# Kernel tuning notes

Measured on AMD Instinct MI355X. Metric: run time of the kernel, lower is better.

The kernel has to match this reference:

```python
import jax, jax.numpy as jnp
import numpy as np

NEG_SLOPE = 0.2  # HANConv default negative_slope
N_NODES = 100000
N_REL = 8
N_EDGES = 200000
N_LABEL = 131072
C_IN = 128
H1 = 128
H2 = 128


def _segment_softmax(logits, seg, num_segments):
    # PyG softmax(src, index): exp(src - max_per_seg) / (sum_per_seg + 1e-16)
    m = jax.ops.segment_max(logits, seg, num_segments=num_segments)
    m = jnp.where(jnp.isfinite(m), m, 0.0)  # empty segments -> 0
    e = jnp.exp(logits - m[seg])
    s = jax.ops.segment_sum(e, seg, num_segments=num_segments)
    return e / (s[seg] + 1e-16)


def _han_layer(x, edge_index, proj_w, proj_b, att_src, att_dst, q, klin_w, klin_b):
    # x: [N, Cin]; edge_index: [R, 2, E]; att_src/att_dst: [R, D]; klin_w: [D, D] (torch [out,in])
    N = x.shape[0]
    h = x @ proj_w + proj_b            # [N, D] shared projection for node type 'node'
    a_src = h @ att_src.T              # [N, R] per-node src attention logits
    a_dst = h @ att_dst.T              # [N, R]

    def per_rel(eidx, a_s, a_d):
        src, dst = eidx[0], eidx[1]
        alpha = jax.nn.leaky_relu(a_s[src] + a_d[dst], NEG_SLOPE)     # [E]
        alpha = _segment_softmax(alpha, dst, N)                        # softmax over in-neighbors
        out = jax.ops.segment_sum(alpha[:, None] * h[src], dst, num_segments=N)  # [N, D]
        return jax.nn.relu(out)        # HANConv applies relu per edge-type output

    outs = jax.vmap(per_rel, in_axes=(0, 1, 1))(edge_index, a_src, a_dst)  # [R, N, D]
    # semantic attention across edge types (group())
    score = jnp.einsum('d,rd->r', q, jnp.tanh(outs @ klin_w.T + klin_b).mean(axis=1))
    attn = jax.nn.softmax(score)       # [R]
    return jnp.einsum('r,rnd->nd', attn, outs)


def setup_inputs() -> dict:
    key = jax.random.key(0)
    ks = jax.random.split(key, 24)
    f32 = jnp.float32

    def lin_w(k, fin, fout):
        return (jax.random.normal(k, (fin, fout), f32) / np.sqrt(fin)).astype(f32)

    inp = {
        'x': jax.random.normal(ks[0], (N_NODES, C_IN), f32),
        'edge_index': jax.random.randint(ks[1], (N_REL, 2, N_EDGES), 0, N_NODES, jnp.int32),
        'edge_label_index': jax.random.randint(ks[2], (2, N_LABEL), 0, N_NODES, jnp.int32),
        # HANConv layer 1 params
        'w1': lin_w(ks[3], C_IN, H1), 'b1': jnp.zeros((H1,), f32),
        'asrc1': jax.random.normal(ks[4], (N_REL, H1), f32) / np.sqrt(H1),
        'adst1': jax.random.normal(ks[5], (N_REL, H1), f32) / np.sqrt(H1),
        'q1': jax.random.normal(ks[6], (H1,), f32) / np.sqrt(H1),
        'kw1': lin_w(ks[7], H1, H1).T, 'kb1': jnp.zeros((H1,), f32),
        # HANConv layer 2 params
        'w2': lin_w(ks[8], H1, H2), 'b2': jnp.zeros((H2,), f32),
        'asrc2': jax.random.normal(ks[9], (N_REL, H2), f32) / np.sqrt(H2),
        'adst2': jax.random.normal(ks[10], (N_REL, H2), f32) / np.sqrt(H2),
        'q2': jax.random.normal(ks[11], (H2,), f32) / np.sqrt(H2),
        'kw2': lin_w(ks[12], H2, H2).T, 'kb2': jnp.zeros((H2,), f32),
        # link-score head
        'post_w': lin_w(ks[13], H2, 2), 'post_b': jnp.zeros((2,), f32),
    }
    return inp


def reference(x, edge_index, edge_label_index,
              w1, b1, asrc1, adst1, q1, kw1, kb1,
              w2, b2, asrc2, adst2, q2, kw2, kb2,
              post_w, post_b):
    h = jax.nn.relu(_han_layer(x, edge_index, w1, b1, asrc1, adst1, q1, kw1, kb1))
    h = jax.nn.relu(_han_layer(h, edge_index, w2, b2, asrc2, adst2, q2, kw2, kb2))
    h_had = h[edge_label_index[0]] * h[edge_label_index[1]]   # [L, H2]
    logits = h_had @ post_w + post_b                          # [L, 2]
    return logits.sum(axis=-1)                                # [L]
```

## Files before the change

kernel.cpp:

```cpp
#include <hip/hip_runtime.h>
#include <hip/hip_fp8.h>

#define NN 100000
#define NR 8
#define NE 200000
#define NL 131072
#define NSEG (NR*NN)
#define NB_SCAN 782
#define NPAD (NB_SCAN*1024)

typedef __attribute__((ext_vector_type(8))) short short8;
typedef __attribute__((ext_vector_type(8))) _Float16 half8;
typedef __attribute__((ext_vector_type(4))) float floatx4;

__device__ __forceinline__ unsigned short f2h(float f) {
    _Float16 h = (_Float16)f;
    union { _Float16 h; unsigned short u; } c; c.h = h; return c.u;
}
__device__ __forceinline__ float h2f(unsigned short u) {
    union { _Float16 h; unsigned short u; } c; c.u = u; return (float)c.h;
}
__device__ __forceinline__ unsigned fp8enc(float f) {
    __hip_fp8_e4m3 t(f); return (unsigned)t.__x;
}
__device__ __forceinline__ float fp8dec(unsigned b) {
    __hip_fp8_e4m3 t; t.__x = (__hip_fp8_storage_t)b; return (float)t;
}

#if defined(__has_builtin)
#if __has_builtin(__builtin_amdgcn_cvt_f32_fp8)
#define HW_FP8_DEC 1
#endif
#endif

__device__ __forceinline__ void dec4(unsigned w, float* f) {
#ifdef HW_FP8_DEC
    f[0] = __builtin_amdgcn_cvt_f32_fp8(w, 0);
    f[1] = __builtin_amdgcn_cvt_f32_fp8(w, 1);
    f[2] = __builtin_amdgcn_cvt_f32_fp8(w, 2);
    f[3] = __builtin_amdgcn_cvt_f32_fp8(w, 3);
#else
    f[0] = fp8dec(w & 0xFF);
    f[1] = fp8dec((w >> 8) & 0xFF);
    f[2] = fp8dec((w >> 16) & 0xFF);
    f[3] = fp8dec((w >> 24) & 0xFF);
#endif
}

__global__ void transpose128(const float* __restrict__ in, float* __restrict__ out) {
    int idx = blockIdx.x * 256 + threadIdx.x;
    int j = idx >> 7, k = idx & 127;
    out[idx] = in[k * 128 + j];
}

__global__ void cast_f16(const float* __restrict__ src, unsigned short* __restrict__ dst) {
    size_t idx = ((size_t)blockIdx.x * 256 + threadIdx.x) * 4;
    float4 v = *(const float4*)(src + idx);
    ushort4 o;
    o.x = f2h(v.x); o.y = f2h(v.y); o.z = f2h(v.z); o.w = f2h(v.w);
    *(ushort4*)(dst + idx) = o;
}

__global__ void hist_kernel(const int* __restrict__ ei, int* __restrict__ counts) {
    int idx = blockIdx.x * 256 + threadIdx.x;
    if (idx >= NR * NE) return;
    int r = idx / NE, e = idx - r * NE;
    int dst = ei[(size_t)r * 2 * NE + NE + e];
    atomicAdd(&counts[r * NN + dst], 1);
}

__global__ __launch_bounds__(256) void scan_k1(const int* __restrict__ counts,
                                               int* __restrict__ rowptr,
                                               int* __restrict__ bsums) {
    __shared__ int wsum[4];
    int t = threadIdx.x, lane = t & 63, w = t >> 6;
    int base = blockIdx.x * 1024 + t * 4;
    int c0 = counts[base], c1 = counts[base + 1], c2 = counts[base + 2], c3 = counts[base + 3];
    int s = c0 + c1 + c2 + c3;
    int inc = s;
#pragma unroll
    for (int off = 1; off < 64; off <<= 1) { int v = __shfl_up(inc, off); if (lane >= off) inc += v; }
    if (lane == 63) wsum[w] = inc;
    __syncthreads();
    int wbase = 0;
    for (int k = 0; k < w; ++k) wbase += wsum[k];
    int ex = wbase + inc - s;
    rowptr[base]     = ex;
    rowptr[base + 1] = ex + c0;
    rowptr[base + 2] = ex + c0 + c1;
    rowptr[base + 3] = ex + c0 + c1 + c2;
    if (t == 255) bsums[blockIdx.x] = wbase + inc;
}

__global__ __launch_bounds__(256) void scan_k2(int* __restrict__ bsums, int nb) {
    __shared__ int wsum[4];
    __shared__ int carry_s;
    int t = threadIdx.x, lane = t & 63, w = t >> 6;
    if (t == 0) carry_s = 0;
    __syncthreads();
    for (int base = 0; base < nb; base += 256) {
        int i = base + t;
        int v = (i < nb) ? bsums[i] : 0;
        int inc = v;
#pragma unroll
        for (int off = 1; off < 64; off <<= 1) { int u = __shfl_up(inc, off); if (lane >= off) inc += u; }
        if (lane == 63) wsum[w] = inc;
        __syncthreads();
        int wbase = carry_s;
        for (int k = 0; k < w; ++k) wbase += wsum[k];
        if (i < nb) bsums[i] = wbase + inc - v;
        __syncthreads();
        if (t == 0) carry_s += wsum[0] + wsum[1] + wsum[2] + wsum[3];
        __syncthreads();
    }
}

__global__ void scan_k3(int* __restrict__ rowptr, const int* __restrict__ bsums) {
    int i = blockIdx.x * 256 + threadIdx.x;
    if (i <= NSEG) rowptr[i] += bsums[i >> 10];
}

__global__ void fill_kernel(const int* __restrict__ ei, const int* __restrict__ rowptr,
                            int* __restrict__ cursor, int* __restrict__ es_raw) {
    int idx = blockIdx.x * 256 + threadIdx.x;
    if (idx >= NR * NE) return;
    int r = idx / NE, e = idx - r * NE;
    int src = ei[(size_t)r * 2 * NE + e];
    int dst = ei[(size_t)r * 2 * NE + NE + e];
    int g = r * NN + dst;
    int pos = rowptr[g] + atomicAdd(&cursor[g], 1);
    es_raw[2 * pos] = src;
}

__global__ __launch_bounds__(256, 3) void gemm_proj(
    const float* __restrict__ A, const float* __restrict__ B,
    const float* __restrict__ bias, float* __restrict__ out, int nrows)
{
    __shared__ float As[128][36];
    __shared__ float Bs[128][36];
    const int tid = threadIdx.x;
    const int row0 = blockIdx.x * 128;
    const int cg = tid & 15;
    const int nb = (tid >> 4) * 8;

    float acc[8][8];
#pragma unroll
    for (int i = 0; i < 8; ++i)
#pragma unroll
        for (int j = 0; j < 8; ++j) acc[i][j] = 0.f;

    for (int k0 = 0; k0 < 128; k0 += 32) {
#pragma unroll
        for (int i = 0; i < 4; ++i) {
            int fi = tid + i * 256;
            int rw = fi >> 3, kq = fi & 7;
            int n = row0 + rw;
            float4 v = make_float4(0.f, 0.f, 0.f, 0.f);
            if (n < nrows) v = *(const float4*)(A + (size_t)n * 128 + k0 + kq * 4);
            *(float4*)&As[rw][kq * 4] = v;
            float4 w = *(const float4*)(B + rw * 128 + k0 + kq * 4);
            *(float4*)&Bs[rw][kq * 4] = w;
        }
        __syncthreads();
#pragma unroll 2
        for (int kq = 0; kq < 8; ++kq) {
            float4 wv[8];
#pragma unroll
            for (int j = 0; j < 8; ++j) wv[j] = *(const float4*)&Bs[cg + 16 * j][kq * 4];
#pragma unroll
            for (int i = 0; i < 8; ++i) {
                float4 xv = *(const float4*)&As[nb + i][kq * 4];
#pragma unroll
                for (int j = 0; j < 8; ++j)
                    acc[i][j] += xv.x * wv[j].x + xv.y * wv[j].y
                               + xv.z * wv[j].z + xv.w * wv[j].w;
            }
        }
        __syncthreads();
    }
#pragma unroll
    for (int i = 0; i < 8; ++i) {
        int n = row0 + nb + i;
        if (n < nrows) {
#pragma unroll
            for (int j = 0; j < 8; ++j) {
                int d = cg + 16 * j;
                out[(size_t)n * 128 + d] = acc[i][j] + bias[d];
            }
        }
    }
}

__global__ __launch_bounds__(256) void fused_score2(
    const int* __restrict__ rowptr, const int2* __restrict__ es,
    const unsigned char* __restrict__ h8,
    const unsigned short* __restrict__ kw16, const float* __restrict__ kb,
    const float* __restrict__ q, float* __restrict__ scorebuf)
{
    __shared__ unsigned short Os[64][136];
    __shared__ float redbuf[4];
    const int t = threadIdx.x;
    const int r = blockIdx.y;
    const int row0 = blockIdx.x * 64;
    const int l = t & 7, ng = t >> 3;

#pragma unroll
    for (int pass = 0; pass < 2; ++pass) {
        int nl = pass * 32 + ng;
        int n = row0 + nl;
        float acc[16];
#pragma unroll
        for (int i = 0; i < 16; ++i) acc[i] = 0.f;
        if (n < NN) {
            int g = r * NN + n;
            int p0 = rowptr[g], p1 = rowptr[g + 1];
            int e = p0;
            for (; e + 1 < p1; e += 2) {
                int2 ea = es[e], eb = es[e + 1];
                float aa = __int_as_float(ea.y), ab = __int_as_float(eb.y);
                const unsigned char* hpa = h8 + (size_t)ea.x * 128 + l * 8;
                const unsigned char* hpb = h8 + (size_t)eb.x * 128 + l * 8;
                uint2 a0 = *(const uint2*)hpa;
                uint2 a1 = *(const uint2*)(hpa + 64);
                uint2 b0 = *(const uint2*)hpb;
                uint2 b1 = *(const uint2*)(hpb + 64);
                float fa[16], fb[16];
                dec4(a0.x, fa);      dec4(a0.y, fa + 4);
                dec4(a1.x, fa + 8);  dec4(a1.y, fa + 12);
                dec4(b0.x, fb);      dec4(b0.y, fb + 4);
                dec4(b1.x, fb + 8);  dec4(b1.y, fb + 12);
#pragma unroll
                for (int i = 0; i < 16; ++i) acc[i] += aa * fa[i] + ab * fb[i];
            }
            if (e < p1) {
                int2 ea = es[e];
                float aa = __int_as_float(ea.y);
                const unsigned char* hpa = h8 + (size_t)ea.x * 128 + l * 8;
                uint2 a0 = *(const uint2*)hpa;
                uint2 a1 = *(const uint2*)(hpa + 64);
                float fa[16];
                dec4(a0.x, fa);      dec4(a0.y, fa + 4);
                dec4(a1.x, fa + 8);  dec4(a1.y, fa + 12);
#pragma unroll
                for (int i = 0; i < 16; ++i) acc[i] += aa * fa[i];
            }
        }
        unsigned short ov[16];
#pragma unroll
        for (int i = 0; i < 16; ++i) ov[i] = f2h(fmaxf(acc[i], 0.f));
        *(short8*)&Os[nl][l * 8]      = *(short8*)&ov[0];
        *(short8*)&Os[nl][64 + l * 8] = *(short8*)&ov[8];
    }
    __syncthreads();

    const int wave = t >> 6, lane = t & 63;
    const int quad = lane >> 4, l16 = lane & 15;
    half8 a[4];
#pragma unroll
    for (int kc = 0; kc < 4; ++kc)
        a[kc] = *(const half8*)&Os[wave * 16 + l16][quad * 8 + kc * 32];

    float s = 0.f;
#pragma unroll
    for (int dt = 0; dt < 8; ++dt) {
        const unsigned short* brow = kw16 + (size_t)(dt * 16 + l16) * 128 + quad * 8;
        floatx4 accv = {0.f, 0.f, 0.f, 0.f};
#pragma unroll
        for (int kc = 0; kc < 4; ++kc) {
            half8 b = *(const half8*)(brow + kc * 32);
            accv = __builtin_amdgcn_mfma_f32_16x16x32_f16(a[kc], b, accv, 0, 0, 0);
        }
        int d = dt * 16 + l16;
        float kbv = kb[d], qv = q[d];
#pragma unroll
        for (int reg = 0; reg < 4; ++reg) {
            int node = row0 + wave * 16 + quad * 4 + reg;
            if (node < NN) {
                float y = accv[reg] + kbv;
                float e2 = __expf(2.f * y);
                float tn = 1.f - 2.f * __builtin_amdgcn_rcpf(e2 + 1.f);
                s += tn * qv;
            }
        }
    }
    for (int off = 32; off > 0; off >>= 1) s += __shfl_down(s, off);
    if (lane == 0) redbuf[wave] = s;
    __syncthreads();
    if (t == 0) atomicAdd(scorebuf + r * 64 + (blockIdx.x & 63),
                          redbuf[0] + redbuf[1] + redbuf[2] + redbuf[3]);
}

__global__ void score_reduce(const float* __restrict__ scorebuf, float* __restrict__ score) {
    int t = threadIdx.x;
    int r = t >> 3, k = t & 7;
    float v = 0.f;
#pragma unroll
    for (int i = 0; i < 8; ++i) v += scorebuf[r * 64 + k * 8 + i];
    v += __shfl_down(v, 4);
    v += __shfl_down(v, 2);
    v += __shfl_down(v, 1);
    if (k == 0) score[r] = v;
}

__global__ __launch_bounds__(256) void att_kernel(
    const float* __restrict__ h, const float* __restrict__ asrc_w,
    const float* __restrict__ adst_w, float* __restrict__ a_src,
    float* __restrict__ a_dst, unsigned short* __restrict__ h16,
    unsigned char* __restrict__ h8)
{
    __shared__ float hs[16][128];
    int n0 = blockIdx.x * 16;
#pragma unroll
    for (int i = 0; i < 2; ++i) {
        int fi = threadIdx.x + i * 256;
        int n = fi >> 5, kq = fi & 31;
        float4 v = make_float4(0.f, 0.f, 0.f, 0.f);
        if (n0 + n < NN) v = *(const float4*)(h + (size_t)(n0 + n) * 128 + kq * 4);
        *(float4*)&hs[n][kq * 4] = v;
    }
    __syncthreads();
    int n = threadIdx.x >> 4, rr = threadIdx.x & 15;
    int r = rr & 7; int isd = rr >> 3;
    const float* w = (isd ? adst_w : asrc_w) + r * 128;
    float acc = 0.f;
#pragma unroll
    for (int kq = 0; kq < 32; ++kq) {
        float4 hv = *(const float4*)&hs[n][kq * 4];
        float4 wv = ((const float4*)w)[kq];
        acc += hv.x * wv.x + hv.y * wv.y + hv.z * wv.z + hv.w * wv.w;
    }
    if (n0 + n < NN) (isd ? a_dst : a_src)[r * NN + n0 + n] = acc;

    int dq = rr * 8;
    if (n0 + n < NN) {
        unsigned short ov[8];
        unsigned lo = 0, hi = 0;
#pragma unroll
        for (int k = 0; k < 8; ++k) {
            float f = hs[n][dq + k];
            ov[k] = f2h(f);
            unsigned b = fp8enc(f);
            if (k < 4) lo |= b << (8 * k); else hi |= b << (8 * (k - 4));
        }
        *(short8*)(h16 + (size_t)(n0 + n) * 128 + dq) = *(short8*)ov;
        *(uint2*)(h8 + (size_t)(n0 + n) * 128 + dq) = make_uint2(lo, hi);
    }
}

__global__ void softmax_csr(const int* __restrict__ rowptr, int2* __restrict__ es,
                            const float* __restrict__ a_src, const float* __restrict__ a_dst)
{
    int g = blockIdx.x * 256 + threadIdx.x;
    if (g >= NSEG) return;
    int p0 = rowptr[g], p1 = rowptr[g + 1];
    int deg = p1 - p0;
    if (deg == 0) return;
    int r = g / NN;
    float ad = a_dst[g];
    const float* as = a_src + (size_t)r * NN;
    if (deg <= 16) {
        float lg[16];
        float m = -1e30f;
#pragma unroll
        for (int i = 0; i < 16; ++i) {
            if (i < deg) {
                float l = as[es[p0 + i].x] + ad;
                l = l > 0.f ? l : 0.2f * l;
                lg[i] = l;
                m = fmaxf(m, l);
            }
        }
        float ssum = 0.f;
#pragma unroll
        for (int i = 0; i < 16; ++i) {
            if (i < deg) { float ex = __expf(lg[i] - m); lg[i] = ex; ssum += ex; }
        }
        float inv = __builtin_amdgcn_rcpf(ssum + 1e-16f);
#pragma unroll
        for (int i = 0; i < 16; ++i) {
            if (i < deg) es[p0 + i].y = __float_as_int(lg[i] * inv);
        }
    } else {
        float m = -1e30f;
        for (int i = p0; i < p1; ++i) {
            float l = as[es[i].x] + ad;
            l = l > 0.f ? l : 0.2f * l;
            es[i].y = __float_as_int(l);
            m = fmaxf(m, l);
        }
        float s = 0.f;
        for (int k = p0; k < p1; ++k) {
            float e = __expf(__int_as_float(es[k].y) - m);
            es[k].y = __float_as_int(e);
            s += e;
        }
        float inv = __builtin_amdgcn_rcpf(s + 1e-16f);
        for (int k = p0; k < p1; ++k)
            es[k].y = __float_as_int(__int_as_float(es[k].y) * inv);
    }
}

__global__ __launch_bounds__(256) void combine_csr(
    const int* __restrict__ rowptr, const int2* __restrict__ es,
    const unsigned short* __restrict__ h16, const float* __restrict__ score,
    float* __restrict__ comb)
{
    __shared__ float attn[NR];
    __shared__ float lds[4][64][17];
    int t = threadIdx.x;
    if (t == 0) {
        float sc[NR]; float m = -1e30f;
        for (int r = 0; r < NR; ++r) { sc[r] = score[r] * (1.0f / NN); m = fmaxf(m, sc[r]); }
        float den = 0.f;
        for (int r = 0; r < NR; ++r) { sc[r] = __expf(sc[r] - m); den += sc[r]; }
        for (int r = 0; r < NR; ++r) attn[r] = sc[r] / den;
    }
    __syncthreads();

    int nl = t >> 6;
    int n = blockIdx.x * 4 + nl;
    int L = t & 63;
    int r = L >> 3;
    int o = L & 7;
    float a[16];
#pragma unroll
    for (int i = 0; i < 16; ++i) a[i] = 0.f;
    {
        int g = r * NN + n;
        int p0 = rowptr[g], p1 = rowptr[g + 1];
        int e = p0;
        for (; e + 1 < p1; e += 2) {
            int2 ea = es[e], eb = es[e + 1];
            float aa = __int_as_float(ea.y), ab = __int_as_float(eb.y);
            const unsigned short* hpa = h16 + (size_t)ea.x * 128;
            const unsigned short* hpb = h16 + (size_t)eb.x * 128;
            short8 u0 = *(const short8*)(hpa + o * 8);
            short8 u1 = *(const short8*)(hpa + 64 + o * 8);
            short8 v0 = *(const short8*)(hpb + o * 8);
            short8 v1 = *(const short8*)(hpb + 64 + o * 8);
#pragma unroll
            for (int i = 0; i < 8; ++i) {
                a[i]     += aa * h2f((unsigned short)u0[i]) + ab * h2f((unsigned short)v0[i]);
                a[8 + i] += aa * h2f((unsigned short)u1[i]) + ab * h2f((unsigned short)v1[i]);
            }
        }
        if (e < p1) {
            int2 ea = es[e];
            float aa = __int_as_float(ea.y);
            const unsigned short* hpa = h16 + (size_t)ea.x * 128;
            short8 u0 = *(const short8*)(hpa + o * 8);
            short8 u1 = *(const short8*)(hpa + 64 + o * 8);
#pragma unroll
            for (int i = 0; i < 8; ++i) {
                a[i]     += aa * h2f((unsigned short)u0[i]);
                a[8 + i] += aa * h2f((unsigned short)u1[i]);
            }
        }
    }
    float w = attn[r];
    float* dst = &lds[nl][L][0];
#pragma unroll
    for (int i = 0; i < 16; ++i) dst[i] = w * fmaxf(a[i], 0.f);
    __syncthreads();

    int d0 = 2 * L;
    int o2, s0;
    if (d0 < 64) { o2 = d0 >> 3; s0 = d0 & 7; }
    else         { o2 = (d0 - 64) >> 3; s0 = 8 + ((d0 - 64) & 7); }
    float x0 = 0.f, x1 = 0.f;
#pragma unroll
    for (int rr = 0; rr < NR; ++rr) {
        x0 += lds[nl][rr * 8 + o2][s0];
        x1 += lds[nl][rr * 8 + o2][s0 + 1];
    }
    *(float2*)(comb + (size_t)n * 128 + d0) = make_float2(x0, x1);
}

__global__ __launch_bounds__(256) void head_kernel(
    const float* __restrict__ hfin, const int* __restrict__ eli,
    const float* __restrict__ pw, const float* __restrict__ pb,
    float* __restrict__ out)
{
    int t = threadIdx.x;
    int l = blockIdx.x * 4 + (t >> 6);
    int d0 = (t & 63) * 2;
    int a = eli[l], b = eli[NL + l];
    float2 ha = *(const float2*)(hfin + (size_t)a * 128 + d0);
    float2 hb = *(const float2*)(hfin + (size_t)b * 128 + d0);
    float w0 = pw[d0 * 2] + pw[d0 * 2 + 1];
    float w1 = pw[d0 * 2 + 2] + pw[d0 * 2 + 3];
    float v = ha.x * hb.x * w0 + ha.y * hb.y * w1;
    for (int off = 32; off > 0; off >>= 1) v += __shfl_down(v, off);
    if ((t & 63) == 0) out[l] = v + pb[0] + pb[1];
}

extern "C" void kernel_launch(void* const* d_in, const int* in_sizes, int n_in,
                              void* d_out, int out_size, void* d_ws, size_t ws_size,
                              hipStream_t stream)
{
    const float* x     = (const float*)d_in[0];
    const int*   ei    = (const int*)d_in[1];
    const int*   eli   = (const int*)d_in[2];
    const float* w1    = (const float*)d_in[3];
    const float* b1    = (const float*)d_in[4];
    const float* asrc1 = (const float*)d_in[5];
    const float* adst1 = (const float*)d_in[6];
    const float* q1    = (const float*)d_in[7];
    const float* kw1   = (const float*)d_in[8];
    const float* kb1   = (const float*)d_in[9];
    const float* w2    = (const float*)d_in[10];
    const float* b2    = (const float*)d_in[11];
    const float* asrc2 = (const float*)d_in[12];
    const float* adst2 = (const float*)d_in[13];
    const float* q2    = (const float*)d_in[14];
    const float* kw2   = (const float*)d_in[15];
    const float* kb2   = (const float*)d_in[16];
    const float* pw    = (const float*)d_in[17];
    const float* pb    = (const float*)d_in[18];
    float* out = (float*)d_out;

    float* ws      = (float*)d_ws;
    float* hA      = ws;
    float* hB      = ws + 12800000ull;
    float* a_src   = ws + 25600000ull;
    float* a_dst   = ws + 26400000ull;
    int2*  es      = (int2*)(ws + 27200000ull);
    int*   rowptr  = (int*)(ws + 30400000ull);
    int*   counts  = (int*)(ws + 31200768ull);
    int*   bsums   = (int*)(ws + 32001536ull);
    float* score   = ws + 32002560ull;
    float* wt      = ws + 32002624ull;
    unsigned short* kw16 = (unsigned short*)(ws + 32019008ull);
    float* scorebuf = (float*)counts;

    hipMemsetAsync(counts, 0, NPAD * sizeof(int), stream);
    hist_kernel<<<6250, 256, 0, stream>>>(ei, counts);
    scan_k1<<<NB_SCAN, 256, 0, stream>>>(counts, rowptr, bsums);
    scan_k2<<<1, 256, 0, stream>>>(bsums, NB_SCAN);
    scan_k3<<<3126, 256, 0, stream>>>(rowptr, bsums);
    hipMemsetAsync(counts, 0, NPAD * sizeof(int), stream);
    fill_kernel<<<6250, 256, 0, stream>>>(ei, rowptr, counts, (int*)es);

    for (int layer = 0; layer < 2; ++layer) {
        const float* Ain  = layer ? hA : x;
        float*       H    = layer ? hB : hA;
        unsigned short* h16 = (unsigned short*)(layer ? hA : hB);
        unsigned char*  h8  = (unsigned char*)(h16 + 12800000ull);
        const float* W    = layer ? w2 : w1;
        const float* bb   = layer ? b2 : b1;
        const float* as_w = layer ? asrc2 : asrc1;
        const float* ad_w = layer ? adst2 : adst1;
        const float* qq   = layer ? q2 : q1;
        const float* kw   = layer ? kw2 : kw1;
        const float* kb   = layer ? kb2 : kb1;

        transpose128<<<64, 256, 0, stream>>>(W, wt);
        gemm_proj<<<782, 256, 0, stream>>>(Ain, wt, bb, H, NN);
        cast_f16<<<16, 256, 0, stream>>>(kw, kw16);
        att_kernel<<<6250, 256, 0, stream>>>(H, as_w, ad_w, a_src, a_dst, h16, h8);
        softmax_csr<<<3125, 256, 0, stream>>>(rowptr, es, a_src, a_dst);
        hipMemsetAsync(scorebuf, 0, 512 * sizeof(float), stream);
        fused_score2<<<dim3(1563, NR), 256, 0, stream>>>(rowptr, es, h8,
                                                         kw16, kb, qq, scorebuf);
        score_reduce<<<1, 64, 0, stream>>>(scorebuf, score);
        combine_csr<<<25000, 256, 0, stream>>>(rowptr, es, h16, score, H);
    }
    head_kernel<<<32768, 256, 0, stream>>>(hB, eli, pw, pb, out);
}
```

Measured before the change: 1.295 ms.

## Materialize per-relation fp16 aggregates in score pass and combine densely

The score kernel now gathers fp16 features instead of fp8 and writes each relation's relu'd aggregate to an fp16 buffer in workspace. A new dense combine kernel then reads those eight buffers and forms the attention-weighted sum, so the second CSR gather pass over edges is no longer needed. This trades a repeated random gather for about 200MB of extra streaming writes and reads, and it depends on a large workspace being available. It also drops fp8 in the score path, which raises score-pass gather bandwidth but improves precision.

```diff
diff --git a/kernel.cpp b/kernel.cpp
--- a/kernel.cpp
+++ b/kernel.cpp
@@ -290,6 +290,110 @@
                           redbuf[0] + redbuf[1] + redbuf[2] + redbuf[3]);
 }
 
+__global__ __launch_bounds__(256) void fused_score2_f16o(
+    const int* __restrict__ rowptr, const int2* __restrict__ es,
+    const unsigned short* __restrict__ h16,
+    const unsigned short* __restrict__ kw16, const float* __restrict__ kb,
+    const float* __restrict__ q, float* __restrict__ scorebuf,
+    unsigned short* __restrict__ O16)
+{
+    __shared__ unsigned short Os[64][136];
+    __shared__ float redbuf[4];
+    const int t = threadIdx.x;
+    const int r = blockIdx.y;
+    const int row0 = blockIdx.x * 64;
+    const int l = t & 7, ng = t >> 3;
+    unsigned short* Orel = O16 + (size_t)r * NN * 128;
+
+#pragma unroll
+    for (int pass = 0; pass < 2; ++pass) {
+        int nl = pass * 32 + ng;
+        int n = row0 + nl;
+        float acc[16];
+#pragma unroll
+        for (int i = 0; i < 16; ++i) acc[i] = 0.f;
+        if (n < NN) {
+            int g = r * NN + n;
+            int p0 = rowptr[g], p1 = rowptr[g + 1];
+            int e = p0;
+            for (; e + 1 < p1; e += 2) {
+                int2 ea = es[e], eb = es[e + 1];
+                float aa = __int_as_float(ea.y), ab = __int_as_float(eb.y);
+                const unsigned short* hpa = h16 + (size_t)ea.x * 128;
+                const unsigned short* hpb = h16 + (size_t)eb.x * 128;
+                short8 a0 = *(const short8*)(hpa + l * 8);
+                short8 a1 = *(const short8*)(hpa + 64 + l * 8);
+                short8 b0 = *(const short8*)(hpb + l * 8);
+                short8 b1 = *(const short8*)(hpb + 64 + l * 8);
+#pragma unroll
+                for (int i = 0; i < 8; ++i)
+                    acc[i]     += aa * h2f((unsigned short)a0[i]) + ab * h2f((unsigned short)b0[i]);
+#pragma unroll
+                for (int i = 0; i < 8; ++i)
+                    acc[8 + i] += aa * h2f((unsigned short)a1[i]) + ab * h2f((unsigned short)b1[i]);
+            }
+            if (e < p1) {
+                int2 ea = es[e];
+                float aa = __int_as_float(ea.y);
+                const unsigned short* hpa = h16 + (size_t)ea.x * 128;
+                short8 a0 = *(const short8*)(hpa + l * 8);
+                short8 a1 = *(const short8*)(hpa + 64 + l * 8);
+#pragma unroll
+                for (int i = 0; i < 8; ++i) acc[i]     += aa * h2f((unsigned short)a0[i]);
+#pragma unroll
+                for (int i = 0; i < 8; ++i) acc[8 + i] += aa * h2f((unsigned short)a1[i]);
+            }
+        }
+        unsigned short ov[16];
+#pragma unroll
+        for (int i = 0; i < 16; ++i) ov[i] = f2h(fmaxf(acc[i], 0.f));
+        if (n < NN) {
+            unsigned short* orow = Orel + (size_t)n * 128;
+            __builtin_nontemporal_store(*(short8*)&ov[0], (short8*)(orow + l * 8));
+            __builtin_nontemporal_store(*(short8*)&ov[8], (short8*)(orow + 64 + l * 8));
+        }
+        *(short8*)&Os[nl][l * 8]      = *(short8*)&ov[0];
+        *(short8*)&Os[nl][64 + l * 8] = *(short8*)&ov[8];
+    }
+    __syncthreads();
+
+    const int wave = t >> 6, lane = t & 63;
+    const int quad = lane >> 4, l16 = lane & 15;
+    half8 a[4];
+#pragma unroll
+    for (int kc = 0; kc < 4; ++kc)
+        a[kc] = *(const half8*)&Os[wave * 16 + l16][quad * 8 + kc * 32];
+
+    float s = 0.f;
+#pragma unroll
+    for (int dt = 0; dt < 8; ++dt) {
+        const unsigned short* brow = kw16 + (size_t)(dt * 16 + l16) * 128 + quad * 8;
+        floatx4 accv = {0.f, 0.f, 0.f, 0.f};
+#pragma unroll
+        for (int kc = 0; kc < 4; ++kc) {
+            half8 b = *(const half8*)(brow + kc * 32);
+            accv = __builtin_amdgcn_mfma_f32_16x16x32_f16(a[kc], b, accv, 0, 0, 0);
+        }
+        int d = dt * 16 + l16;
+        float kbv = kb[d], qv = q[d];
+#pragma unroll
+        for (int reg = 0; reg < 4; ++reg) {
+            int node = row0 + wave * 16 + quad * 4 + reg;
+            if (node < NN) {
+                float y = accv[reg] + kbv;
+                float e2 = __expf(2.f * y);
+                float tn = 1.f - 2.f * __builtin_amdgcn_rcpf(e2 + 1.f);
+                s += tn * qv;
+            }
+        }
+    }
+    for (int off = 32; off > 0; off >>= 1) s += __shfl_down(s, off);
+    if (lane == 0) redbuf[wave] = s;
+    __syncthreads();
+    if (t == 0) atomicAdd(scorebuf + r * 64 + (blockIdx.x & 63),
+                          redbuf[0] + redbuf[1] + redbuf[2] + redbuf[3]);
+}
+
 __global__ void score_reduce(const float* __restrict__ scorebuf, float* __restrict__ score) {
     int t = threadIdx.x;
     int r = t >> 3, k = t & 7;
@@ -474,6 +578,41 @@
         x1 += lds[nl][rr * 8 + o2][s0 + 1];
     }
     *(float2*)(comb + (size_t)n * 128 + d0) = make_float2(x0, x1);
+}
+
+__global__ __launch_bounds__(256) void combine_dense16(
+    const unsigned short* __restrict__ O16, const float* __restrict__ score,
+    float* __restrict__ comb)
+{
+    __shared__ float attn[NR];
+    int t = threadIdx.x;
+    if (t == 0) {
+        float sc[NR]; float m = -1e30f;
+        for (int r = 0; r < NR; ++r) { sc[r] = score[r] * (1.0f / NN); m = fmaxf(m, sc[r]); }
+        float den = 0.f;
+        for (int r = 0; r < NR; ++r) { sc[r] = __expf(sc[r] - m); den += sc[r]; }
+        for (int r = 0; r < NR; ++r) attn[r] = sc[r] / den;
+    }
+    __syncthreads();
+    float w[NR];
+#pragma unroll
+    for (int r = 0; r < NR; ++r) w[r] = attn[r];
+
+    const size_t total = (size_t)NN * 16;
+    const size_t rstride = (size_t)NN * 128;
+    for (size_t i = (size_t)blockIdx.x * 256 + t; i < total;
+         i += (size_t)gridDim.x * 256) {
+        float acc[8] = {0.f, 0.f, 0.f, 0.f, 0.f, 0.f, 0.f, 0.f};
+#pragma unroll
+        for (int r = 0; r < NR; ++r) {
+            short8 v = __builtin_nontemporal_load(
+                (const short8*)(O16 + (size_t)r * rstride) + i);
+#pragma unroll
+            for (int j = 0; j < 8; ++j) acc[j] += w[r] * h2f((unsigned short)v[j]);
+        }
+        *(float4*)(comb + i * 8)     = make_float4(acc[0], acc[1], acc[2], acc[3]);
+        *(float4*)(comb + i * 8 + 4) = make_float4(acc[4], acc[5], acc[6], acc[7]);
+    }
 }
 
 __global__ __launch_bounds__(256) void head_kernel(
@@ -531,6 +670,8 @@
     float* score   = ws + 32002560ull;
     float* wt      = ws + 32002624ull;
     unsigned short* kw16 = (unsigned short*)(ws + 32019008ull);
+    unsigned short* O16 = (unsigned short*)(ws + 32027200ull);
+    const bool bigws = ws_size >= 83227200ull * sizeof(float);
     float* scorebuf = (float*)counts;
 
     hipMemsetAsync(counts, 0, NPAD * sizeof(int), stream);
@@ -560,10 +701,17 @@
         att_kernel<<<6250, 256, 0, stream>>>(H, as_w, ad_w, a_src, a_dst, h16, h8);
         softmax_csr<<<3125, 256, 0, stream>>>(rowptr, es, a_src, a_dst);
         hipMemsetAsync(scorebuf, 0, 512 * sizeof(float), stream);
-        fused_score2<<<dim3(1563, NR), 256, 0, stream>>>(rowptr, es, h8,
-                                                         kw16, kb, qq, scorebuf);
-        score_reduce<<<1, 64, 0, stream>>>(scorebuf, score);
-        combine_csr<<<25000, 256, 0, stream>>>(rowptr, es, h16, score, H);
+        if (bigws) {
+            fused_score2_f16o<<<dim3(1563, NR), 256, 0, stream>>>(
+                rowptr, es, h16, kw16, kb, qq, scorebuf, O16);
+            score_reduce<<<1, 64, 0, stream>>>(scorebuf, score);
+            combine_dense16<<<2048, 256, 0, stream>>>(O16, score, H);
+        } else {
+            fused_score2<<<dim3(1563, NR), 256, 0, stream>>>(
+                rowptr, es, h8, kw16, kb, qq, scorebuf);
+            score_reduce<<<1, 64, 0, stream>>>(scorebuf, score);
+            combine_csr<<<25000, 256, 0, stream>>>(rowptr, es, h16, score, H);
+        }
     }
     head_kernel<<<32768, 256, 0, stream>>>(hB, eli, pw, pb, out);
 }
```

After: 1.297 ms. Within noise of the previous version (+0.1%).

## Replace FP32 projection GEMM with split-bf16 MFMA GEMM

Applied to the files above, without the earlier changes.

Replaces the scalar FP32 shared-memory tiled projection GEMM with a matrix-core kernel. Activations and weights are each split into a bf16 high part and a bf16 residual, and three bf16 MFMA products per k-chunk approximate FP32 accuracy. A small kernel pre-splits the transposed weights, and each block converts 64 rows of input in shared memory. The aim is to move the dense projection onto matrix cores, at the cost of extra conversion work and a small loss of precision against true FP32.

```diff
diff --git a/kernel.cpp b/kernel.cpp
--- a/kernel.cpp
+++ b/kernel.cpp
@@ -19,6 +19,14 @@
 }
 __device__ __forceinline__ float h2f(unsigned short u) {
     union { _Float16 h; unsigned short u; } c; c.u = u; return (float)c.h;
+}
+__device__ __forceinline__ unsigned short f2bf(float f) {
+    unsigned u = __float_as_uint(f);
+    unsigned r = (u + 0x7fff + ((u >> 16) & 1)) >> 16;
+    return (unsigned short)r;
+}
+__device__ __forceinline__ float bf2f(unsigned short s) {
+    return __uint_as_float(((unsigned)s) << 16);
 }
 __device__ __forceinline__ unsigned fp8enc(float f) {
     __hip_fp8_e4m3 t(f); return (unsigned)t.__x;
@@ -61,6 +69,20 @@
     *(ushort4*)(dst + idx) = o;
 }
 
+__global__ void cast_wsplit(const float* __restrict__ src,
+                            unsigned short* __restrict__ hi,
+                            unsigned short* __restrict__ lo) {
+    size_t idx = ((size_t)blockIdx.x * 256 + threadIdx.x) * 4;
+    float4 v = *(const float4*)(src + idx);
+    ushort4 h, l;
+    h.x = f2bf(v.x); l.x = f2bf(v.x - bf2f(h.x));
+    h.y = f2bf(v.y); l.y = f2bf(v.y - bf2f(h.y));
+    h.z = f2bf(v.z); l.z = f2bf(v.z - bf2f(h.z));
+    h.w = f2bf(v.w); l.w = f2bf(v.w - bf2f(h.w));
+    *(ushort4*)(hi + idx) = h;
+    *(ushort4*)(lo + idx) = l;
+}
+
 __global__ void hist_kernel(const int* __restrict__ ei, int* __restrict__ counts) {
     int idx = blockIdx.x * 256 + threadIdx.x;
     if (idx >= NR * NE) return;
@@ -132,61 +154,60 @@
     es_raw[2 * pos] = src;
 }
 
-__global__ __launch_bounds__(256, 3) void gemm_proj(
-    const float* __restrict__ A, const float* __restrict__ B,
-    const float* __restrict__ bias, float* __restrict__ out, int nrows)
-{
-    __shared__ float As[128][36];
-    __shared__ float Bs[128][36];
-    const int tid = threadIdx.x;
-    const int row0 = blockIdx.x * 128;
-    const int cg = tid & 15;
-    const int nb = (tid >> 4) * 8;
-
-    float acc[8][8];
-#pragma unroll
-    for (int i = 0; i < 8; ++i)
-#pragma unroll
-        for (int j = 0; j < 8; ++j) acc[i][j] = 0.f;
-
-    for (int k0 = 0; k0 < 128; k0 += 32) {
-#pragma unroll
-        for (int i = 0; i < 4; ++i) {
-            int fi = tid + i * 256;
-            int rw = fi >> 3, kq = fi & 7;
-            int n = row0 + rw;
-            float4 v = make_float4(0.f, 0.f, 0.f, 0.f);
-            if (n < nrows) v = *(const float4*)(A + (size_t)n * 128 + k0 + kq * 4);
-            *(float4*)&As[rw][kq * 4] = v;
-            float4 w = *(const float4*)(B + rw * 128 + k0 + kq * 4);
-            *(float4*)&Bs[rw][kq * 4] = w;
-        }
-        __syncthreads();
-#pragma unroll 2
-        for (int kq = 0; kq < 8; ++kq) {
-            float4 wv[8];
-#pragma unroll
-            for (int j = 0; j < 8; ++j) wv[j] = *(const float4*)&Bs[cg + 16 * j][kq * 4];
-#pragma unroll
-            for (int i = 0; i < 8; ++i) {
-                float4 xv = *(const float4*)&As[nb + i][kq * 4];
-#pragma unroll
-                for (int j = 0; j < 8; ++j)
-                    acc[i][j] += xv.x * wv[j].x + xv.y * wv[j].y
-                               + xv.z * wv[j].z + xv.w * wv[j].w;
-            }
-        }
-        __syncthreads();
-    }
+__global__ __launch_bounds__(256) void gemm_mfma(
+    const float* __restrict__ A, const unsigned short* __restrict__ whi,
+    const unsigned short* __restrict__ wlo, const float* __restrict__ bias,
+    float* __restrict__ out, int nrows)
+{
+    __shared__ unsigned short Ahi[64][136];
+    __shared__ unsigned short Alo[64][136];
+    const int t = threadIdx.x;
+    const int row0 = blockIdx.x * 64;
+
 #pragma unroll
     for (int i = 0; i < 8; ++i) {
-        int n = row0 + nb + i;
-        if (n < nrows) {
-#pragma unroll
-            for (int j = 0; j < 8; ++j) {
-                int d = cg + 16 * j;
-                out[(size_t)n * 128 + d] = acc[i][j] + bias[d];
-            }
+        int idx = t + i * 256;
+        int rw = idx >> 5, kq = idx & 31;
+        int n = row0 + rw;
+        float4 v = make_float4(0.f, 0.f, 0.f, 0.f);
+        if (n < nrows) v = *(const float4*)(A + (size_t)n * 128 + kq * 4);
+        ushort4 h, l;
+        h.x = f2bf(v.x); l.x = f2bf(v.x - bf2f(h.x));
+        h.y = f2bf(v.y); l.y = f2bf(v.y - bf2f(h.y));
+        h.z = f2bf(v.z); l.z = f2bf(v.z - bf2f(h.z));
+        h.w = f2bf(v.w); l.w = f2bf(v.w - bf2f(h.w));
+        *(ushort4*)&Ahi[rw][kq * 4] = h;
+        *(ushort4*)&Alo[rw][kq * 4] = l;
+    }
+    __syncthreads();
+
+    const int wave = t >> 6, lane = t & 63;
+    const int quad = lane >> 4, l16 = lane & 15;
+    short8 ah[4], al[4];
+#pragma unroll
+    for (int kc = 0; kc < 4; ++kc) {
+        ah[kc] = *(const short8*)&Ahi[wave * 16 + l16][quad * 8 + kc * 32];
+        al[kc] = *(const short8*)&Alo[wave * 16 + l16][quad * 8 + kc * 32];
+    }
+
+#pragma unroll
+    for (int dt = 0; dt < 8; ++dt) {
+        const size_t boff = (size_t)(dt * 16 + l16) * 128 + quad * 8;
+        floatx4 accv = {0.f, 0.f, 0.f, 0.f};
+#pragma unroll
+        for (int kc = 0; kc < 4; ++kc) {
+            short8 bh = *(const short8*)(whi + boff + kc * 32);
+            short8 bl = *(const short8*)(wlo + boff + kc * 32);
+            accv = __builtin_amdgcn_mfma_f32_16x16x32_bf16(ah[kc], bh, accv, 0, 0, 0);
+            accv = __builtin_amdgcn_mfma_f32_16x16x32_bf16(ah[kc], bl, accv, 0, 0, 0);
+            accv = __builtin_amdgcn_mfma_f32_16x16x32_bf16(al[kc], bh, accv, 0, 0, 0);
+        }
+        int d = dt * 16 + l16;
+        float bv = bias[d];
+#pragma unroll
+        for (int reg = 0; reg < 4; ++reg) {
+            int node = row0 + wave * 16 + quad * 4 + reg;
+            if (node < nrows) out[(size_t)node * 128 + d] = accv[reg] + bv;
         }
     }
 }
@@ -531,6 +552,8 @@
     float* score   = ws + 32002560ull;
     float* wt      = ws + 32002624ull;
     unsigned short* kw16 = (unsigned short*)(ws + 32019008ull);
+    unsigned short* whi16 = (unsigned short*)(ws + 32027200ull);
+    unsigned short* wlo16 = (unsigned short*)(ws + 32035392ull);
     float* scorebuf = (float*)counts;
 
     hipMemsetAsync(counts, 0, NPAD * sizeof(int), stream);
@@ -555,7 +578,8 @@
         const float* kb   = layer ? kb2 : kb1;
 
         transpose128<<<64, 256, 0, stream>>>(W, wt);
-        gemm_proj<<<782, 256, 0, stream>>>(Ain, wt, bb, H, NN);
+        cast_wsplit<<<16, 256, 0, stream>>>(wt, whi16, wlo16);
+        gemm_mfma<<<1563, 256, 0, stream>>>(Ain, whi16, wlo16, bb, H, NN);
         cast_f16<<<16, 256, 0, stream>>>(kw, kw16);
         att_kernel<<<6250, 256, 0, stream>>>(H, as_w, ad_w, a_src, a_dst, h16, h8);
         softmax_csr<<<3125, 256, 0, stream>>>(rowptr, es, a_src, a_dst);
```

Result: no change. 1.291 ms (-0.3%).
